# Optimization experiments

Measured on AMD Instinct MI355X. Metric: run time of the kernel, lower is better.

The kernel has to match this reference:

```python
import jax, jax.numpy as jnp
import numpy as np

F_IN = 22 * 1000   # flattened EEG trial
D_DENSE = 100      # Dense(100) -> becomes T=100 timesteps of dim 1
H = 128            # LSTM units
N_CLASS = 4


def setup_inputs() -> dict:
    key = jax.random.key(0)
    ks = jax.random.split(key, 8)
    B = 4096
    s1 = 1.0 / np.sqrt(F_IN)
    sr = 1.0 / np.sqrt(H)
    x = jax.random.normal(ks[0], (B, 22, 1000), dtype=jnp.float32)
    W1 = jax.random.uniform(ks[1], (F_IN, D_DENSE), jnp.float32, -s1, s1)
    b1 = jnp.zeros((D_DENSE,), jnp.float32)
    # Keras LSTM kernels: input kernel [1, 4H], recurrent kernel [H, 4H], bias [4H]
    Wk = jax.random.uniform(ks[2], (1, 4 * H), jnp.float32, -1.0, 1.0)
    Wr = jax.random.normal(ks[3], (H, 4 * H), dtype=jnp.float32) * sr
    # Keras unit_forget_bias: f-gate bias initialized to 1
    bl = jnp.concatenate([jnp.zeros(H), jnp.ones(H), jnp.zeros(2 * H)]).astype(jnp.float32)
    W2 = jax.random.uniform(ks[4], (H, N_CLASS), jnp.float32, -sr, sr)
    b2 = jnp.zeros((N_CLASS,), jnp.float32)
    return {"x": x, "W1": W1, "b1": b1, "Wk": Wk, "Wr": Wr, "bl": bl, "W2": W2, "b2": b2}


def _lstm_last(seq, Wk, Wr, bl):
    # seq: [B, T, 1]; returns final hidden state [B, H]
    B = seq.shape[0]
    # precompute input contribution for all steps: [T, B, 4H]
    zx = jnp.einsum('btf,fg->tbg', seq, Wk) + bl

    def step(carry, zxt):
        h, c = carry
        z = zxt + h @ Wr                      # [B, 4H]
        i, f, g, o = jnp.split(z, 4, axis=-1)  # keras gate order: i, f, c, o
        i = jax.nn.sigmoid(i)
        f = jax.nn.sigmoid(f)
        g = jnp.tanh(g)
        o = jax.nn.sigmoid(o)
        c = f * c + i * g
        h = o * jnp.tanh(c)
        return (h, c), None

    init = (jnp.zeros((B, H), seq.dtype), jnp.zeros((B, H), seq.dtype))
    (h, _), _ = jax.lax.scan(step, init, zx)
    return h


def reference(x, W1, b1, Wk, Wr, bl, W2, b2):
    B = x.shape[0]
    flat = x.reshape(B, -1)                 # Flatten
    d = flat @ W1 + b1                      # Dense(100), linear activation
    seq = d.reshape(B, D_DENSE, 1)          # Reshape((100, 1))
    h = _lstm_last(seq, Wk, Wr, bl)         # LSTM(128) -> last hidden state
    logits = h @ W2 + b2                    # Dense(4)
    return jax.nn.softmax(logits, axis=-1)
```

## Files before the change

### kernel.cpp

```cpp
#include <hip/hip_runtime.h>
#include <stdint.h>

#define F_IN   22000
#define B_SZ   4096
#define T_STEPS 100
#define NSPLIT 16
#define NCHUNK 22
#define KSPAN  (NCHUNK * 64)
#define ACC_STRIDE 104
#define ACCB_BYTES ((size_t)B_SZ * ACC_STRIDE * 4)
#define BIMG_BYTES 28672
#define BIMG_HALF  14336
#define W1IMG_BYTES ((size_t)NSPLIT * NCHUNK * BIMG_BYTES)
#define WRIMG_BYTES (128 * 1024)

typedef float f32x4 __attribute__((ext_vector_type(4)));
typedef short s16x8 __attribute__((ext_vector_type(8)));

__device__ inline unsigned short f2bf(float f){
  unsigned u = __builtin_bit_cast(unsigned, f);
  u += 0x7FFFu + ((u >> 16) & 1u);
  return (unsigned short)(u >> 16);
}
__device__ inline float bf2f(unsigned short h){
  return __builtin_bit_cast(float, ((unsigned)h) << 16);
}
__device__ inline float sigf(float x){
  return __builtin_amdgcn_rcpf(1.f + __expf(-x));
}
__device__ inline float tanhf_(float x){
  return 1.f - 2.f * __builtin_amdgcn_rcpf(__expf(2.f * x) + 1.f);
}

__global__ __launch_bounds__(256) void k_zero(float4* __restrict__ p, int n4){
  int i = blockIdx.x * 256 + threadIdx.x;
  if (i < n4) p[i] = make_float4(0.f, 0.f, 0.f, 0.f);
}

__global__ __launch_bounds__(256) void k_w1img(const float* __restrict__ W1,
                                               char* __restrict__ img){
  __shared__ float tile[64][129];
  int ch = blockIdx.x, s = blockIdx.y;
  int k0 = s * KSPAN + ch * 64;
  char* base = img + ((size_t)(s * NCHUNK + ch)) * BIMG_BYTES;
  int tid = threadIdx.x;
  for (int idx = tid; idx < 64 * 128; idx += 256){
    int k = idx >> 7, c = idx & 127;
    float v = 0.f;
    if (c < 100 && (k0 + k) < F_IN) v = W1[(size_t)(k0 + k) * 100 + c];
    tile[k][c] = v;
  }
  __syncthreads();
  #pragma unroll
  for (int q = 0; q < 4; ++q){
    int task = q * 256 + tid;
    if (task < 896){
      int p  = task * 16;
      int c  = p >> 7;
      int k8 = ((p >> 4) & 7) ^ (c & 7);
      unsigned hw[4], lw[4];
      #pragma unroll
      for (int jj = 0; jj < 4; ++jj){
        float v0 = tile[k8 * 8 + jj * 2][c];
        float v1 = tile[k8 * 8 + jj * 2 + 1][c];
        unsigned short h0 = f2bf(v0), l0 = f2bf(v0 - bf2f(h0));
        unsigned short h1 = f2bf(v1), l1 = f2bf(v1 - bf2f(h1));
        hw[jj] = (unsigned)h0 | ((unsigned)h1 << 16);
        lw[jj] = (unsigned)l0 | ((unsigned)l1 << 16);
      }
      *(uint4*)(base + p)             = make_uint4(hw[0], hw[1], hw[2], hw[3]);
      *(uint4*)(base + BIMG_HALF + p) = make_uint4(lw[0], lw[1], lw[2], lw[3]);
    }
  }
}

__global__ __launch_bounds__(256) void k_wrimg(const float* __restrict__ Wr,
                                               char* __restrict__ wrimg){
  int gid = blockIdx.x * 256 + threadIdx.x;
  int lane = gid & 63, slot = gid >> 6;
  int kk = slot & 3, G = (slot >> 2) & 3, w = slot >> 4;
  int oct = lane >> 4, lr = lane & 15;
  int col = G * 128 + w * 16 + lr;
  unsigned pk[4];
  #pragma unroll
  for (int jj = 0; jj < 4; ++jj){
    float v0 = Wr[(size_t)(kk * 32 + oct * 8 + jj * 2)     * 512 + col];
    float v1 = Wr[(size_t)(kk * 32 + oct * 8 + jj * 2 + 1) * 512 + col];
    pk[jj] = (unsigned)f2bf(v0) | ((unsigned)f2bf(v1) << 16);
  }
  *(uint4*)(wrimg + (size_t)gid * 16) = make_uint4(pk[0], pk[1], pk[2], pk[3]);
}

__global__ __launch_bounds__(256, 2) void k_dense(const float* __restrict__ x,
                                                  const char* __restrict__ img,
                                                  float* __restrict__ accb){
  __shared__ char Bb0[BIMG_BYTES], Bb1[BIMG_BYTES];
  int tid = threadIdx.x;
  int lane = tid & 63, w = tid >> 6;
  int r = lane & 15, oct = lane >> 4;
  int brow = blockIdx.x * 64;
  int s = blockIdx.y;
  int arow = brow + w * 16 + r;
  const float* xrow = x + (size_t)arow * F_IN;
  const char* isrc = img + (size_t)s * NCHUNK * BIMG_BYTES;
  int kbase = s * KSPAN;

  f32x4 acc[7];
  #pragma unroll
  for (int i = 0; i < 7; ++i) acc[i] = (f32x4)0.f;

  float4 xa0, xa1, xa2, xa3;
  float4 ya0, ya1, ya2, ya3;

#define ALOAD(CH, A0, A1, A2, A3) do{                                        \
    int k0_ = kbase + (CH) * 64;                                             \
    int ka0_ = k0_ + oct * 8;                                                \
    int ka1_ = k0_ + 32 + oct * 8;                                           \
    A0 = make_float4(0.f,0.f,0.f,0.f); A1 = A0; A2 = A0; A3 = A0;            \
    if (ka0_ < F_IN){ A0 = *(const float4*)(xrow + ka0_);                    \
                      A1 = *(const float4*)(xrow + ka0_ + 4); }              \
    if (ka1_ < F_IN){ A2 = *(const float4*)(xrow + ka1_);                    \
                      A3 = *(const float4*)(xrow + ka1_ + 4); }              \
  }while(0)

#define STAGE(CH, BUF) do{                                                   \
    const char* src_ = isrc + (size_t)(CH) * BIMG_BYTES;                     \
    _Pragma("unroll")                                                        \
    for (int i_ = 0; i_ < 7; ++i_){                                          \
      int seg_ = i_ * 4 + w;                                                 \
      __builtin_amdgcn_global_load_lds(                                      \
        (const __attribute__((address_space(1))) void*)(src_ + seg_ * 1024 + lane * 16), \
        (__attribute__((address_space(3))) void*)((BUF) + seg_ * 1024), 16, 0, 0); \
    }                                                                        \
  }while(0)

#define CONVMFMA(BUF, A0, A1, A2, A3) do{                                    \
    float va_[16] = {A0.x,A0.y,A0.z,A0.w, A1.x,A1.y,A1.z,A1.w,               \
                     A2.x,A2.y,A2.z,A2.w, A3.x,A3.y,A3.z,A3.w};              \
    s16x8 ah0_, al0_, ah1_, al1_;                                            \
    _Pragma("unroll")                                                        \
    for (int j_ = 0; j_ < 8; ++j_){                                          \
      unsigned short h_ = f2bf(va_[j_]);                                     \
      ah0_[j_] = (short)h_; al0_[j_] = (short)f2bf(va_[j_] - bf2f(h_));      \
    }                                                                        \
    _Pragma("unroll")                                                        \
    for (int j_ = 0; j_ < 8; ++j_){                                          \
      unsigned short h_ = f2bf(va_[8 + j_]);                                 \
      ah1_[j_] = (short)h_; al1_[j_] = (short)f2bf(va_[8 + j_] - bf2f(h_));  \
    }                                                                        \
    _Pragma("unroll")                                                        \
    for (int ct_ = 0; ct_ < 7; ++ct_){                                       \
      int c_ = ct_ * 16 + r;                                                 \
      int byte0_ = ((c_ * 128 + oct * 16) ^ ((c_ & 7) << 4));                \
      int byte1_ = ((c_ * 128 + 64 + oct * 16) ^ ((c_ & 7) << 4));           \
      s16x8 bh0_ = *(s16x8*)((BUF) + byte0_);                                \
      s16x8 bl0_ = *(s16x8*)((BUF) + BIMG_HALF + byte0_);                    \
      s16x8 bh1_ = *(s16x8*)((BUF) + byte1_);                                \
      s16x8 bl1_ = *(s16x8*)((BUF) + BIMG_HALF + byte1_);                    \
      acc[ct_] = __builtin_amdgcn_mfma_f32_16x16x32_bf16(ah0_, bh0_, acc[ct_], 0, 0, 0); \
      acc[ct_] = __builtin_amdgcn_mfma_f32_16x16x32_bf16(ah0_, bl0_, acc[ct_], 0, 0, 0); \
      acc[ct_] = __builtin_amdgcn_mfma_f32_16x16x32_bf16(al0_, bh0_, acc[ct_], 0, 0, 0); \
      acc[ct_] = __builtin_amdgcn_mfma_f32_16x16x32_bf16(ah1_, bh1_, acc[ct_], 0, 0, 0); \
      acc[ct_] = __builtin_amdgcn_mfma_f32_16x16x32_bf16(ah1_, bl1_, acc[ct_], 0, 0, 0); \
      acc[ct_] = __builtin_amdgcn_mfma_f32_16x16x32_bf16(al1_, bh1_, acc[ct_], 0, 0, 0); \
    }                                                                        \
  }while(0)

  STAGE(0, Bb0);
  ALOAD(0, xa0, xa1, xa2, xa3);
  __syncthreads();

  for (int ch = 0; ch < NCHUNK; ch += 2){
    if (ch + 1 < NCHUNK){
      STAGE(ch + 1, Bb1);
      ALOAD(ch + 1, ya0, ya1, ya2, ya3);
    }
    CONVMFMA(Bb0, xa0, xa1, xa2, xa3);
    __syncthreads();
    if (ch + 1 < NCHUNK){
      if (ch + 2 < NCHUNK){
        STAGE(ch + 2, Bb0);
        ALOAD(ch + 2, xa0, xa1, xa2, xa3);
      }
      CONVMFMA(Bb1, ya0, ya1, ya2, ya3);
      __syncthreads();
    }
  }

#undef ALOAD
#undef STAGE
#undef CONVMFMA

  #pragma unroll
  for (int ct = 0; ct < 7; ++ct){
    int col = ct * 16 + r;
    if (col < 100){
      #pragma unroll
      for (int reg = 0; reg < 4; ++reg){
        int orow = brow + w * 16 + oct * 4 + reg;
        atomicAdd(&accb[(size_t)orow * ACC_STRIDE + col], acc[ct][reg]);
      }
    }
  }
}

__global__ __launch_bounds__(512, 2) void k_lstm(const float* __restrict__ accb,
                                                 const float* __restrict__ b1,
                                                 const float* __restrict__ Wk,
                                                 const char* __restrict__ wrimg,
                                                 const float* __restrict__ bl,
                                                 const float* __restrict__ W2,
                                                 const float* __restrict__ b2,
                                                 float* __restrict__ out){
  __shared__ unsigned short hbuf[2][16 * 128];
  __shared__ float dld[16][ACC_STRIDE];
  __shared__ float hf[16][132];
  int tid = threadIdx.x;
  int lane = tid & 63, w = tid >> 6;
  int oct = lane >> 4, lr = lane & 15;
  int brow = blockIdx.x * 16;

  for (int i = tid; i < 2048; i += 512) hbuf[0][i] = 0;
  for (int i = tid; i < 16 * T_STEPS; i += 512){
    int r = i / T_STEPS, t = i % T_STEPS;
    dld[r][t] = accb[(size_t)(brow + r) * ACC_STRIDE + t] + b1[t];
  }

  float wkv[4], blv[4];
  s16x8 bfrag[4][4];
  #pragma unroll
  for (int G = 0; G < 4; ++G){
    int col = G * 128 + w * 16 + lr;
    wkv[G] = Wk[col];
    blv[G] = bl[col];
    #pragma unroll
    for (int kk = 0; kk < 4; ++kk){
      bfrag[G][kk] = *(const s16x8*)(wrimg +
          ((size_t)(((w * 4 + G) * 4 + kk) * 64 + lane)) * 16);
    }
  }
  float cst[4];
  #pragma unroll
  for (int reg = 0; reg < 4; ++reg) cst[reg] = 0.f;
  __syncthreads();

  for (int t = 0; t < T_STEPS; ++t){
    int cur = t & 1;
    f32x4 acc[4];
    float dv[4];
    #pragma unroll
    for (int reg = 0; reg < 4; ++reg) dv[reg] = dld[oct * 4 + reg][t];
    #pragma unroll
    for (int G = 0; G < 4; ++G)
      #pragma unroll
      for (int reg = 0; reg < 4; ++reg)
        acc[G][reg] = dv[reg] * wkv[G] + blv[G];
    #pragma unroll
    for (int kk = 0; kk < 4; ++kk){
      int abyte = (lr * 256 + kk * 64 + oct * 16) ^ ((lr & 7) << 4);
      s16x8 a = *(s16x8*)((char*)hbuf[cur] + abyte);
      #pragma unroll
      for (int G = 0; G < 4; ++G)
        acc[G] = __builtin_amdgcn_mfma_f32_16x16x32_bf16(a, bfrag[G][kk], acc[G], 0, 0, 0);
    }
    #pragma unroll
    for (int reg = 0; reg < 4; ++reg){
      float iv = sigf(acc[0][reg]);
      float fv = sigf(acc[1][reg]);
      float gv = tanhf_(acc[2][reg]);
      float ov = sigf(acc[3][reg]);
      float cv = fv * cst[reg] + iv * gv;
      cst[reg] = cv;
      float hv = ov * tanhf_(cv);
      int row = oct * 4 + reg;
      int col = w * 16 + lr;
      int byte = (row * 256 + col * 2) ^ ((row & 7) << 4);
      *(unsigned short*)((char*)hbuf[cur ^ 1] + byte) = f2bf(hv);
      if (t == T_STEPS - 1) hf[row][col] = hv;
    }
    __syncthreads();
  }

  if (tid < 64){
    int row = tid >> 2, cl = tid & 3;
    float a = b2[cl];
    #pragma unroll 8
    for (int j = 0; j < 128; ++j) a += hf[row][j] * W2[j * 4 + cl];
    float m = fmaxf(a, __shfl_xor(a, 1));
    m = fmaxf(m, __shfl_xor(m, 2));
    float e = __expf(a - m);
    float se = e + __shfl_xor(e, 1);
    se += __shfl_xor(se, 2);
    out[(size_t)(brow + row) * 4 + cl] = e * __builtin_amdgcn_rcpf(se);
  }
}

extern "C" void kernel_launch(void* const* d_in, const int* in_sizes, int n_in,
                              void* d_out, int out_size, void* d_ws, size_t ws_size,
                              hipStream_t stream){
  const float* x  = (const float*)d_in[0];
  const float* W1 = (const float*)d_in[1];
  const float* b1 = (const float*)d_in[2];
  const float* Wk = (const float*)d_in[3];
  const float* Wr = (const float*)d_in[4];
  const float* bl = (const float*)d_in[5];
  const float* W2 = (const float*)d_in[6];
  const float* b2 = (const float*)d_in[7];
  float* out = (float*)d_out;

  float* accb  = (float*)d_ws;
  char*  img   = (char*)d_ws + ACCB_BYTES;
  char*  wrimg = (char*)d_ws + ACCB_BYTES + W1IMG_BYTES;
  const int n4 = B_SZ * ACC_STRIDE / 4;

  k_zero<<<(n4 + 255) / 256, 256, 0, stream>>>((float4*)accb, n4);
  k_w1img<<<dim3(NCHUNK, NSPLIT), 256, 0, stream>>>(W1, img);
  k_wrimg<<<32, 256, 0, stream>>>(Wr, wrimg);
  k_dense<<<dim3(B_SZ / 64, NSPLIT), 256, 0, stream>>>(x, img, accb);
  k_lstm<<<B_SZ / 16, 512, 0, stream>>>(accb, b1, Wk, wrimg, bl, W2, b2, out);
}
```

Measured before the change: 242.9 us.

## Process two 16-row A tiles per wave in dense GEMM to reuse B fragments

Each wave in k_dense now covers 32 batch rows instead of 16. Every B fragment read from LDS feeds two sets of MFMAs with separate accumulators, and the grid is halved along the batch dimension. The aim is to halve LDS B reads and global image staging per row, and to double MFMA work per sync. In exchange, accumulator and input register use roughly doubles, which may lower occupancy below the launch bound of 2 or cause spills, and the grid now has fewer blocks.

```diff
diff --git a/kernel.cpp b/kernel.cpp
--- a/kernel.cpp
+++ b/kernel.cpp
@@ -98,29 +98,35 @@
   int tid = threadIdx.x;
   int lane = tid & 63, w = tid >> 6;
   int r = lane & 15, oct = lane >> 4;
-  int brow = blockIdx.x * 64;
+  int brow = blockIdx.x * 128;
   int s = blockIdx.y;
-  int arow = brow + w * 16 + r;
-  const float* xrow = x + (size_t)arow * F_IN;
+  int arow0 = brow + w * 32 + r;
+  const float* xrow0 = x + (size_t)arow0 * F_IN;
+  const float* xrow1 = xrow0 + (size_t)16 * F_IN;
   const char* isrc = img + (size_t)s * NCHUNK * BIMG_BYTES;
   int kbase = s * KSPAN;
 
-  f32x4 acc[7];
-  #pragma unroll
-  for (int i = 0; i < 7; ++i) acc[i] = (f32x4)0.f;
-
-  float4 xa0, xa1, xa2, xa3;
-  float4 ya0, ya1, ya2, ya3;
-
-#define ALOAD(CH, A0, A1, A2, A3) do{                                        \
+  f32x4 acc0[7], acc1[7];
+  #pragma unroll
+  for (int i = 0; i < 7; ++i){ acc0[i] = (f32x4)0.f; acc1[i] = (f32x4)0.f; }
+
+  float4 xa0, xa1, xa2, xa3, xb0, xb1, xb2, xb3;
+  float4 ya0, ya1, ya2, ya3, yb0, yb1, yb2, yb3;
+
+#define ALOAD(CH, A0, A1, A2, A3, B0, B1, B2, B3) do{                        \
     int k0_ = kbase + (CH) * 64;                                             \
     int ka0_ = k0_ + oct * 8;                                                \
     int ka1_ = k0_ + 32 + oct * 8;                                           \
     A0 = make_float4(0.f,0.f,0.f,0.f); A1 = A0; A2 = A0; A3 = A0;            \
-    if (ka0_ < F_IN){ A0 = *(const float4*)(xrow + ka0_);                    \
-                      A1 = *(const float4*)(xrow + ka0_ + 4); }              \
-    if (ka1_ < F_IN){ A2 = *(const float4*)(xrow + ka1_);                    \
-                      A3 = *(const float4*)(xrow + ka1_ + 4); }              \
+    B0 = A0; B1 = A0; B2 = A0; B3 = A0;                                      \
+    if (ka0_ < F_IN){ A0 = *(const float4*)(xrow0 + ka0_);                   \
+                      A1 = *(const float4*)(xrow0 + ka0_ + 4);               \
+                      B0 = *(const float4*)(xrow1 + ka0_);                   \
+                      B1 = *(const float4*)(xrow1 + ka0_ + 4); }             \
+    if (ka1_ < F_IN){ A2 = *(const float4*)(xrow0 + ka1_);                   \
+                      A3 = *(const float4*)(xrow0 + ka1_ + 4);               \
+                      B2 = *(const float4*)(xrow1 + ka1_);                   \
+                      B3 = *(const float4*)(xrow1 + ka1_ + 4); }             \
   }while(0)
 
 #define STAGE(CH, BUF) do{                                                   \
@@ -134,20 +140,27 @@
     }                                                                        \
   }while(0)
 
-#define CONVMFMA(BUF, A0, A1, A2, A3) do{                                    \
-    float va_[16] = {A0.x,A0.y,A0.z,A0.w, A1.x,A1.y,A1.z,A1.w,               \
-                     A2.x,A2.y,A2.z,A2.w, A3.x,A3.y,A3.z,A3.w};              \
-    s16x8 ah0_, al0_, ah1_, al1_;                                            \
+#define CONV16(VA, H0, L0, H1, L1) do{                                       \
     _Pragma("unroll")                                                        \
     for (int j_ = 0; j_ < 8; ++j_){                                          \
-      unsigned short h_ = f2bf(va_[j_]);                                     \
-      ah0_[j_] = (short)h_; al0_[j_] = (short)f2bf(va_[j_] - bf2f(h_));      \
+      unsigned short h_ = f2bf(VA[j_]);                                      \
+      H0[j_] = (short)h_; L0[j_] = (short)f2bf(VA[j_] - bf2f(h_));           \
     }                                                                        \
     _Pragma("unroll")                                                        \
     for (int j_ = 0; j_ < 8; ++j_){                                          \
-      unsigned short h_ = f2bf(va_[8 + j_]);                                 \
-      ah1_[j_] = (short)h_; al1_[j_] = (short)f2bf(va_[8 + j_] - bf2f(h_));  \
+      unsigned short h_ = f2bf(VA[8 + j_]);                                  \
+      H1[j_] = (short)h_; L1[j_] = (short)f2bf(VA[8 + j_] - bf2f(h_));       \
     }                                                                        \
+  }while(0)
+
+#define CONVMFMA(BUF, A0, A1, A2, A3, B0, B1, B2, B3) do{                    \
+    float va_[16] = {A0.x,A0.y,A0.z,A0.w, A1.x,A1.y,A1.z,A1.w,               \
+                     A2.x,A2.y,A2.z,A2.w, A3.x,A3.y,A3.z,A3.w};              \
+    float vb_[16] = {B0.x,B0.y,B0.z,B0.w, B1.x,B1.y,B1.z,B1.w,               \
+                     B2.x,B2.y,B2.z,B2.w, B3.x,B3.y,B3.z,B3.w};              \
+    s16x8 pah0_, pal0_, pah1_, pal1_, qah0_, qal0_, qah1_, qal1_;            \
+    CONV16(va_, pah0_, pal0_, pah1_, pal1_);                                 \
+    CONV16(vb_, qah0_, qal0_, qah1_, qal1_);                                 \
     _Pragma("unroll")                                                        \
     for (int ct_ = 0; ct_ < 7; ++ct_){                                       \
       int c_ = ct_ * 16 + r;                                                 \
@@ -157,38 +170,45 @@
       s16x8 bl0_ = *(s16x8*)((BUF) + BIMG_HALF + byte0_);                    \
       s16x8 bh1_ = *(s16x8*)((BUF) + byte1_);                                \
       s16x8 bl1_ = *(s16x8*)((BUF) + BIMG_HALF + byte1_);                    \
-      acc[ct_] = __builtin_amdgcn_mfma_f32_16x16x32_bf16(ah0_, bh0_, acc[ct_], 0, 0, 0); \
-      acc[ct_] = __builtin_amdgcn_mfma_f32_16x16x32_bf16(ah0_, bl0_, acc[ct_], 0, 0, 0); \
-      acc[ct_] = __builtin_amdgcn_mfma_f32_16x16x32_bf16(al0_, bh0_, acc[ct_], 0, 0, 0); \
-      acc[ct_] = __builtin_amdgcn_mfma_f32_16x16x32_bf16(ah1_, bh1_, acc[ct_], 0, 0, 0); \
-      acc[ct_] = __builtin_amdgcn_mfma_f32_16x16x32_bf16(ah1_, bl1_, acc[ct_], 0, 0, 0); \
-      acc[ct_] = __builtin_amdgcn_mfma_f32_16x16x32_bf16(al1_, bh1_, acc[ct_], 0, 0, 0); \
+      acc0[ct_] = __builtin_amdgcn_mfma_f32_16x16x32_bf16(pah0_, bh0_, acc0[ct_], 0, 0, 0); \
+      acc0[ct_] = __builtin_amdgcn_mfma_f32_16x16x32_bf16(pah0_, bl0_, acc0[ct_], 0, 0, 0); \
+      acc0[ct_] = __builtin_amdgcn_mfma_f32_16x16x32_bf16(pal0_, bh0_, acc0[ct_], 0, 0, 0); \
+      acc0[ct_] = __builtin_amdgcn_mfma_f32_16x16x32_bf16(pah1_, bh1_, acc0[ct_], 0, 0, 0); \
+      acc0[ct_] = __builtin_amdgcn_mfma_f32_16x16x32_bf16(pah1_, bl1_, acc0[ct_], 0, 0, 0); \
+      acc0[ct_] = __builtin_amdgcn_mfma_f32_16x16x32_bf16(pal1_, bh1_, acc0[ct_], 0, 0, 0); \
+      acc1[ct_] = __builtin_amdgcn_mfma_f32_16x16x32_bf16(qah0_, bh0_, acc1[ct_], 0, 0, 0); \
+      acc1[ct_] = __builtin_amdgcn_mfma_f32_16x16x32_bf16(qah0_, bl0_, acc1[ct_], 0, 0, 0); \
+      acc1[ct_] = __builtin_amdgcn_mfma_f32_16x16x32_bf16(qal0_, bh0_, acc1[ct_], 0, 0, 0); \
+      acc1[ct_] = __builtin_amdgcn_mfma_f32_16x16x32_bf16(qah1_, bh1_, acc1[ct_], 0, 0, 0); \
+      acc1[ct_] = __builtin_amdgcn_mfma_f32_16x16x32_bf16(qah1_, bl1_, acc1[ct_], 0, 0, 0); \
+      acc1[ct_] = __builtin_amdgcn_mfma_f32_16x16x32_bf16(qal1_, bh1_, acc1[ct_], 0, 0, 0); \
     }                                                                        \
   }while(0)
 
+  ALOAD(0, xa0, xa1, xa2, xa3, xb0, xb1, xb2, xb3);
   STAGE(0, Bb0);
-  ALOAD(0, xa0, xa1, xa2, xa3);
   __syncthreads();
 
   for (int ch = 0; ch < NCHUNK; ch += 2){
     if (ch + 1 < NCHUNK){
+      ALOAD(ch + 1, ya0, ya1, ya2, ya3, yb0, yb1, yb2, yb3);
       STAGE(ch + 1, Bb1);
-      ALOAD(ch + 1, ya0, ya1, ya2, ya3);
-    }
-    CONVMFMA(Bb0, xa0, xa1, xa2, xa3);
+    }
+    CONVMFMA(Bb0, xa0, xa1, xa2, xa3, xb0, xb1, xb2, xb3);
     __syncthreads();
     if (ch + 1 < NCHUNK){
       if (ch + 2 < NCHUNK){
+        ALOAD(ch + 2, xa0, xa1, xa2, xa3, xb0, xb1, xb2, xb3);
         STAGE(ch + 2, Bb0);
-        ALOAD(ch + 2, xa0, xa1, xa2, xa3);
       }
-      CONVMFMA(Bb1, ya0, ya1, ya2, ya3);
+      CONVMFMA(Bb1, ya0, ya1, ya2, ya3, yb0, yb1, yb2, yb3);
       __syncthreads();
     }
   }
 
 #undef ALOAD
 #undef STAGE
+#undef CONV16
 #undef CONVMFMA
 
   #pragma unroll
@@ -197,8 +217,9 @@
     if (col < 100){
       #pragma unroll
       for (int reg = 0; reg < 4; ++reg){
-        int orow = brow + w * 16 + oct * 4 + reg;
-        atomicAdd(&accb[(size_t)orow * ACC_STRIDE + col], acc[ct][reg]);
+        int orow0 = brow + w * 32 + oct * 4 + reg;
+        atomicAdd(&accb[(size_t)orow0 * ACC_STRIDE + col], acc0[ct][reg]);
+        atomicAdd(&accb[(size_t)(orow0 + 16) * ACC_STRIDE + col], acc1[ct][reg]);
       }
     }
   }
@@ -316,6 +337,6 @@
   k_zero<<<(n4 + 255) / 256, 256, 0, stream>>>((float4*)accb, n4);
   k_w1img<<<dim3(NCHUNK, NSPLIT), 256, 0, stream>>>(W1, img);
   k_wrimg<<<32, 256, 0, stream>>>(Wr, wrimg);
-  k_dense<<<dim3(B_SZ / 64, NSPLIT), 256, 0, stream>>>(x, img, accb);
+  k_dense<<<dim3(B_SZ / 128, NSPLIT), 256, 0, stream>>>(x, img, accb);
   k_lstm<<<B_SZ / 16, 512, 0, stream>>>(accb, b1, Wk, wrimg, bl, W2, b2, out);
 }
```

New measurement: 238.4 us. About the same (-1.8%).

## Merge prep kernels into one launch and single-buffer dense LDS for occupancy

Applied to the files above, without the earlier changes.

The three setup kernels (accumulator zeroing, W1 bf16 split image, Wr image) are merged into one block-indexed prep kernel, removing two launches. The dense GEMM kernel drops its double-buffered LDS staging and software prefetch, using a single 28KB buffer with two barriers per chunk, and raises launch bounds to 4 blocks per CU. The goal is to hide latency through more resident waves instead of explicit overlap. The risk is exposed load latency inside each block and extra barriers.

```diff
diff --git a/kernel.cpp b/kernel.cpp
--- a/kernel.cpp
+++ b/kernel.cpp
@@ -12,7 +12,6 @@
 #define BIMG_BYTES 28672
 #define BIMG_HALF  14336
 #define W1IMG_BYTES ((size_t)NSPLIT * NCHUNK * BIMG_BYTES)
-#define WRIMG_BYTES (128 * 1024)
 
 typedef float f32x4 __attribute__((ext_vector_type(4)));
 typedef short s16x8 __attribute__((ext_vector_type(8)));
@@ -32,69 +31,71 @@
   return 1.f - 2.f * __builtin_amdgcn_rcpf(__expf(2.f * x) + 1.f);
 }
 
-__global__ __launch_bounds__(256) void k_zero(float4* __restrict__ p, int n4){
-  int i = blockIdx.x * 256 + threadIdx.x;
-  if (i < n4) p[i] = make_float4(0.f, 0.f, 0.f, 0.f);
-}
-
-__global__ __launch_bounds__(256) void k_w1img(const float* __restrict__ W1,
-                                               char* __restrict__ img){
+__global__ __launch_bounds__(256) void k_prep(const float* __restrict__ W1,
+                                              const float* __restrict__ Wr,
+                                              char* __restrict__ img,
+                                              char* __restrict__ wrimg,
+                                              float4* __restrict__ accb4){
   __shared__ float tile[64][129];
-  int ch = blockIdx.x, s = blockIdx.y;
-  int k0 = s * KSPAN + ch * 64;
-  char* base = img + ((size_t)(s * NCHUNK + ch)) * BIMG_BYTES;
-  int tid = threadIdx.x;
-  for (int idx = tid; idx < 64 * 128; idx += 256){
-    int k = idx >> 7, c = idx & 127;
-    float v = 0.f;
-    if (c < 100 && (k0 + k) < F_IN) v = W1[(size_t)(k0 + k) * 100 + c];
-    tile[k][c] = v;
-  }
-  __syncthreads();
-  #pragma unroll
-  for (int q = 0; q < 4; ++q){
-    int task = q * 256 + tid;
-    if (task < 896){
-      int p  = task * 16;
-      int c  = p >> 7;
-      int k8 = ((p >> 4) & 7) ^ (c & 7);
-      unsigned hw[4], lw[4];
-      #pragma unroll
-      for (int jj = 0; jj < 4; ++jj){
-        float v0 = tile[k8 * 8 + jj * 2][c];
-        float v1 = tile[k8 * 8 + jj * 2 + 1][c];
-        unsigned short h0 = f2bf(v0), l0 = f2bf(v0 - bf2f(h0));
-        unsigned short h1 = f2bf(v1), l1 = f2bf(v1 - bf2f(h1));
-        hw[jj] = (unsigned)h0 | ((unsigned)h1 << 16);
-        lw[jj] = (unsigned)l0 | ((unsigned)l1 << 16);
+  int b = blockIdx.x, tid = threadIdx.x;
+  if (b < 352){
+    int ch = b % NCHUNK, s = b / NCHUNK;
+    int k0 = s * KSPAN + ch * 64;
+    char* base = img + ((size_t)(s * NCHUNK + ch)) * BIMG_BYTES;
+    for (int idx = tid; idx < 64 * 128; idx += 256){
+      int k = idx >> 7, c = idx & 127;
+      float v = 0.f;
+      if (c < 100 && (k0 + k) < F_IN) v = W1[(size_t)(k0 + k) * 100 + c];
+      tile[k][c] = v;
+    }
+    __syncthreads();
+    #pragma unroll
+    for (int q = 0; q < 4; ++q){
+      int task = q * 256 + tid;
+      if (task < 896){
+        int p  = task * 16;
+        int c  = p >> 7;
+        int k8 = ((p >> 4) & 7) ^ (c & 7);
+        unsigned hw[4], lw[4];
+        #pragma unroll
+        for (int jj = 0; jj < 4; ++jj){
+          float v0 = tile[k8 * 8 + jj * 2][c];
+          float v1 = tile[k8 * 8 + jj * 2 + 1][c];
+          unsigned short h0 = f2bf(v0), l0 = f2bf(v0 - bf2f(h0));
+          unsigned short h1 = f2bf(v1), l1 = f2bf(v1 - bf2f(h1));
+          hw[jj] = (unsigned)h0 | ((unsigned)h1 << 16);
+          lw[jj] = (unsigned)l0 | ((unsigned)l1 << 16);
+        }
+        *(uint4*)(base + p)             = make_uint4(hw[0], hw[1], hw[2], hw[3]);
+        *(uint4*)(base + BIMG_HALF + p) = make_uint4(lw[0], lw[1], lw[2], lw[3]);
       }
-      *(uint4*)(base + p)             = make_uint4(hw[0], hw[1], hw[2], hw[3]);
-      *(uint4*)(base + BIMG_HALF + p) = make_uint4(lw[0], lw[1], lw[2], lw[3]);
-    }
-  }
-}
-
-__global__ __launch_bounds__(256) void k_wrimg(const float* __restrict__ Wr,
-                                               char* __restrict__ wrimg){
-  int gid = blockIdx.x * 256 + threadIdx.x;
-  int lane = gid & 63, slot = gid >> 6;
-  int kk = slot & 3, G = (slot >> 2) & 3, w = slot >> 4;
-  int oct = lane >> 4, lr = lane & 15;
-  int col = G * 128 + w * 16 + lr;
-  unsigned pk[4];
-  #pragma unroll
-  for (int jj = 0; jj < 4; ++jj){
-    float v0 = Wr[(size_t)(kk * 32 + oct * 8 + jj * 2)     * 512 + col];
-    float v1 = Wr[(size_t)(kk * 32 + oct * 8 + jj * 2 + 1) * 512 + col];
-    pk[jj] = (unsigned)f2bf(v0) | ((unsigned)f2bf(v1) << 16);
-  }
-  *(uint4*)(wrimg + (size_t)gid * 16) = make_uint4(pk[0], pk[1], pk[2], pk[3]);
-}
-
-__global__ __launch_bounds__(256, 2) void k_dense(const float* __restrict__ x,
+    }
+  } else if (b < 384){
+    int gid = (b - 352) * 256 + tid;
+    int lane = gid & 63, slot = gid >> 6;
+    int kk = slot & 3, G = (slot >> 2) & 3, w = slot >> 4;
+    int oct = lane >> 4, lr = lane & 15;
+    int col = G * 128 + w * 16 + lr;
+    unsigned pk[4];
+    #pragma unroll
+    for (int jj = 0; jj < 4; ++jj){
+      float v0 = Wr[(size_t)(kk * 32 + oct * 8 + jj * 2)     * 512 + col];
+      float v1 = Wr[(size_t)(kk * 32 + oct * 8 + jj * 2 + 1) * 512 + col];
+      pk[jj] = (unsigned)f2bf(v0) | ((unsigned)f2bf(v1) << 16);
+    }
+    *(uint4*)(wrimg + (size_t)gid * 16) = make_uint4(pk[0], pk[1], pk[2], pk[3]);
+  } else {
+    int bb = b - 384;
+    #pragma unroll
+    for (int it = 0; it < 4; ++it)
+      accb4[(size_t)bb * 1024 + it * 256 + tid] = make_float4(0.f, 0.f, 0.f, 0.f);
+  }
+}
+
+__global__ __launch_bounds__(256, 4) void k_dense(const float* __restrict__ x,
                                                   const char* __restrict__ img,
                                                   float* __restrict__ accb){
-  __shared__ char Bb0[BIMG_BYTES], Bb1[BIMG_BYTES];
+  __shared__ char Bb[BIMG_BYTES];
   int tid = threadIdx.x;
   int lane = tid & 63, w = tid >> 6;
   int r = lane & 15, oct = lane >> 4;
@@ -109,87 +110,57 @@
   #pragma unroll
   for (int i = 0; i < 7; ++i) acc[i] = (f32x4)0.f;
 
-  float4 xa0, xa1, xa2, xa3;
-  float4 ya0, ya1, ya2, ya3;
-
-#define ALOAD(CH, A0, A1, A2, A3) do{                                        \
-    int k0_ = kbase + (CH) * 64;                                             \
-    int ka0_ = k0_ + oct * 8;                                                \
-    int ka1_ = k0_ + 32 + oct * 8;                                           \
-    A0 = make_float4(0.f,0.f,0.f,0.f); A1 = A0; A2 = A0; A3 = A0;            \
-    if (ka0_ < F_IN){ A0 = *(const float4*)(xrow + ka0_);                    \
-                      A1 = *(const float4*)(xrow + ka0_ + 4); }              \
-    if (ka1_ < F_IN){ A2 = *(const float4*)(xrow + ka1_);                    \
-                      A3 = *(const float4*)(xrow + ka1_ + 4); }              \
-  }while(0)
-
-#define STAGE(CH, BUF) do{                                                   \
-    const char* src_ = isrc + (size_t)(CH) * BIMG_BYTES;                     \
-    _Pragma("unroll")                                                        \
-    for (int i_ = 0; i_ < 7; ++i_){                                          \
-      int seg_ = i_ * 4 + w;                                                 \
-      __builtin_amdgcn_global_load_lds(                                      \
-        (const __attribute__((address_space(1))) void*)(src_ + seg_ * 1024 + lane * 16), \
-        (__attribute__((address_space(3))) void*)((BUF) + seg_ * 1024), 16, 0, 0); \
-    }                                                                        \
-  }while(0)
-
-#define CONVMFMA(BUF, A0, A1, A2, A3) do{                                    \
-    float va_[16] = {A0.x,A0.y,A0.z,A0.w, A1.x,A1.y,A1.z,A1.w,               \
-                     A2.x,A2.y,A2.z,A2.w, A3.x,A3.y,A3.z,A3.w};              \
-    s16x8 ah0_, al0_, ah1_, al1_;                                            \
-    _Pragma("unroll")                                                        \
-    for (int j_ = 0; j_ < 8; ++j_){                                          \
-      unsigned short h_ = f2bf(va_[j_]);                                     \
-      ah0_[j_] = (short)h_; al0_[j_] = (short)f2bf(va_[j_] - bf2f(h_));      \
-    }                                                                        \
-    _Pragma("unroll")                                                        \
-    for (int j_ = 0; j_ < 8; ++j_){                                          \
-      unsigned short h_ = f2bf(va_[8 + j_]);                                 \
-      ah1_[j_] = (short)h_; al1_[j_] = (short)f2bf(va_[8 + j_] - bf2f(h_));  \
-    }                                                                        \
-    _Pragma("unroll")                                                        \
-    for (int ct_ = 0; ct_ < 7; ++ct_){                                       \
-      int c_ = ct_ * 16 + r;                                                 \
-      int byte0_ = ((c_ * 128 + oct * 16) ^ ((c_ & 7) << 4));                \
-      int byte1_ = ((c_ * 128 + 64 + oct * 16) ^ ((c_ & 7) << 4));           \
-      s16x8 bh0_ = *(s16x8*)((BUF) + byte0_);                                \
-      s16x8 bl0_ = *(s16x8*)((BUF) + BIMG_HALF + byte0_);                    \
-      s16x8 bh1_ = *(s16x8*)((BUF) + byte1_);                                \
-      s16x8 bl1_ = *(s16x8*)((BUF) + BIMG_HALF + byte1_);                    \
-      acc[ct_] = __builtin_amdgcn_mfma_f32_16x16x32_bf16(ah0_, bh0_, acc[ct_], 0, 0, 0); \
-      acc[ct_] = __builtin_amdgcn_mfma_f32_16x16x32_bf16(ah0_, bl0_, acc[ct_], 0, 0, 0); \
-      acc[ct_] = __builtin_amdgcn_mfma_f32_16x16x32_bf16(al0_, bh0_, acc[ct_], 0, 0, 0); \
-      acc[ct_] = __builtin_amdgcn_mfma_f32_16x16x32_bf16(ah1_, bh1_, acc[ct_], 0, 0, 0); \
-      acc[ct_] = __builtin_amdgcn_mfma_f32_16x16x32_bf16(ah1_, bl1_, acc[ct_], 0, 0, 0); \
-      acc[ct_] = __builtin_amdgcn_mfma_f32_16x16x32_bf16(al1_, bh1_, acc[ct_], 0, 0, 0); \
-    }                                                                        \
-  }while(0)
-
-  STAGE(0, Bb0);
-  ALOAD(0, xa0, xa1, xa2, xa3);
-  __syncthreads();
-
-  for (int ch = 0; ch < NCHUNK; ch += 2){
-    if (ch + 1 < NCHUNK){
-      STAGE(ch + 1, Bb1);
-      ALOAD(ch + 1, ya0, ya1, ya2, ya3);
-    }
-    CONVMFMA(Bb0, xa0, xa1, xa2, xa3);
-    __syncthreads();
-    if (ch + 1 < NCHUNK){
-      if (ch + 2 < NCHUNK){
-        STAGE(ch + 2, Bb0);
-        ALOAD(ch + 2, xa0, xa1, xa2, xa3);
+  for (int ch = 0; ch < NCHUNK; ++ch){
+    int k0 = kbase + ch * 64;
+    int ka0 = k0 + oct * 8;
+    int ka1 = k0 + 32 + oct * 8;
+    float4 a0 = make_float4(0.f,0.f,0.f,0.f), a1 = a0, a2 = a0, a3 = a0;
+    if (ka0 < F_IN){ a0 = *(const float4*)(xrow + ka0);
+                     a1 = *(const float4*)(xrow + ka0 + 4); }
+    if (ka1 < F_IN){ a2 = *(const float4*)(xrow + ka1);
+                     a3 = *(const float4*)(xrow + ka1 + 4); }
+    {
+      const char* src = isrc + (size_t)ch * BIMG_BYTES;
+      #pragma unroll
+      for (int i = 0; i < 7; ++i){
+        int seg = i * 4 + w;
+        __builtin_amdgcn_global_load_lds(
+          (const __attribute__((address_space(1))) void*)(src + seg * 1024 + lane * 16),
+          (__attribute__((address_space(3))) void*)(Bb + seg * 1024), 16, 0, 0);
       }
-      CONVMFMA(Bb1, ya0, ya1, ya2, ya3);
-      __syncthreads();
-    }
-  }
-
-#undef ALOAD
-#undef STAGE
-#undef CONVMFMA
+    }
+    __syncthreads();
+    float va[16] = {a0.x,a0.y,a0.z,a0.w, a1.x,a1.y,a1.z,a1.w,
+                    a2.x,a2.y,a2.z,a2.w, a3.x,a3.y,a3.z,a3.w};
+    s16x8 ah0, al0, ah1, al1;
+    #pragma unroll
+    for (int j = 0; j < 8; ++j){
+      unsigned short h = f2bf(va[j]);
+      ah0[j] = (short)h; al0[j] = (short)f2bf(va[j] - bf2f(h));
+    }
+    #pragma unroll
+    for (int j = 0; j < 8; ++j){
+      unsigned short h = f2bf(va[8 + j]);
+      ah1[j] = (short)h; al1[j] = (short)f2bf(va[8 + j] - bf2f(h));
+    }
+    #pragma unroll
+    for (int ct = 0; ct < 7; ++ct){
+      int c = ct * 16 + r;
+      int byte0 = ((c * 128 + oct * 16) ^ ((c & 7) << 4));
+      int byte1 = ((c * 128 + 64 + oct * 16) ^ ((c & 7) << 4));
+      s16x8 bh0 = *(s16x8*)(Bb + byte0);
+      s16x8 bl0 = *(s16x8*)(Bb + BIMG_HALF + byte0);
+      s16x8 bh1 = *(s16x8*)(Bb + byte1);
+      s16x8 bl1 = *(s16x8*)(Bb + BIMG_HALF + byte1);
+      acc[ct] = __builtin_amdgcn_mfma_f32_16x16x32_bf16(ah0, bh0, acc[ct], 0, 0, 0);
+      acc[ct] = __builtin_amdgcn_mfma_f32_16x16x32_bf16(ah0, bl0, acc[ct], 0, 0, 0);
+      acc[ct] = __builtin_amdgcn_mfma_f32_16x16x32_bf16(al0, bh0, acc[ct], 0, 0, 0);
+      acc[ct] = __builtin_amdgcn_mfma_f32_16x16x32_bf16(ah1, bh1, acc[ct], 0, 0, 0);
+      acc[ct] = __builtin_amdgcn_mfma_f32_16x16x32_bf16(ah1, bl1, acc[ct], 0, 0, 0);
+      acc[ct] = __builtin_amdgcn_mfma_f32_16x16x32_bf16(al1, bh1, acc[ct], 0, 0, 0);
+    }
+    __syncthreads();
+  }
 
   #pragma unroll
   for (int ct = 0; ct < 7; ++ct){
@@ -311,11 +282,8 @@
   float* accb  = (float*)d_ws;
   char*  img   = (char*)d_ws + ACCB_BYTES;
   char*  wrimg = (char*)d_ws + ACCB_BYTES + W1IMG_BYTES;
-  const int n4 = B_SZ * ACC_STRIDE / 4;
-
-  k_zero<<<(n4 + 255) / 256, 256, 0, stream>>>((float4*)accb, n4);
-  k_w1img<<<dim3(NCHUNK, NSPLIT), 256, 0, stream>>>(W1, img);
-  k_wrimg<<<32, 256, 0, stream>>>(Wr, wrimg);
+
+  k_prep<<<488, 256, 0, stream>>>(W1, Wr, img, wrimg, (float4*)accb);
   k_dense<<<dim3(B_SZ / 64, NSPLIT), 256, 0, stream>>>(x, img, accb);
   k_lstm<<<B_SZ / 16, 512, 0, stream>>>(accb, b1, Wk, wrimg, bl, W2, b2, out);
 }
```

Result: faster. 234.9 us (-3.3%).
